# Optimization experiments

Measured on AMD Instinct MI355X. Metric: run time of the kernel, lower is better.

Reference implementation:

```python
import jax, jax.numpy as jnp
import numpy as np

B, N, D, L = 4, 256, 512, 3  # batch, seq_len, input_dim, n_layer


def setup_inputs() -> dict:
    key = jax.random.key(0)
    ks = jax.random.split(key, 12)
    s = 0.02
    return {
        "x": jax.random.normal(ks[0], (B, N, D), dtype=jnp.float32),
        # Highway: L layers, each a gate Linear(D,D) and transform Linear(D,D)
        "hw_gate_w": jax.random.normal(ks[1], (L, D, D), dtype=jnp.float32) * s,
        "hw_gate_b": jnp.zeros((L, D), dtype=jnp.float32),
        "hw_tr_w": jax.random.normal(ks[2], (L, D, D), dtype=jnp.float32) * s,
        "hw_tr_b": jnp.zeros((L, D), dtype=jnp.float32),
        # link_weight MLP: Linear(2D,D) -> ReLU -> [Linear(D,D) -> ReLU]*(L-2) -> Linear(D,1) -> Sigmoid
        "lw0_w": jax.random.normal(ks[3], (D, 2 * D), dtype=jnp.float32) * s,
        "lw0_b": jnp.zeros((D,), dtype=jnp.float32),
        "lw1_w": jax.random.normal(ks[4], (D, D), dtype=jnp.float32) * s,
        "lw1_b": jnp.zeros((D,), dtype=jnp.float32),
        "lwo_w": jax.random.normal(ks[5], (1, D), dtype=jnp.float32) * s,
        "lwo_b": jnp.zeros((1,), dtype=jnp.float32),
    }


def _highway(x, gw, gb, tw, tb):
    # standard highway: y = g * relu(Wt x + bt) + (1 - g) * x, g = sigmoid(Wg x + bg)
    for i in range(gw.shape[0]):
        g = jax.nn.sigmoid(jnp.einsum('bnd,ed->bne', x, gw[i]) + gb[i])
        t = jax.nn.relu(jnp.einsum('bnd,ed->bne', x, tw[i]) + tb[i])
        x = g * t + (1.0 - g) * x
    return x


def reference(x, hw_gate_w, hw_gate_b, hw_tr_w, hw_tr_b,
              lw0_w, lw0_b, lw1_w, lw1_b, lwo_w, lwo_b):
    d = x.shape[-1]
    h = _highway(x, hw_gate_w, hw_gate_b, hw_tr_w, hw_tr_b)  # [B,N,D]
    # Fused pairwise-concat + first Linear: cat(h_i, h_j) @ W0.T ==
    # h_i @ W0[:, :D].T + h_j @ W0[:, D:].T  (avoids the [B,N*N,2D] tensor)
    a = jnp.einsum('bnd,ed->bne', h, lw0_w[:, :d])  # uses m1 (row i)
    b = jnp.einsum('bnd,ed->bne', h, lw0_w[:, d:])  # uses m2 (col j)
    z = jax.nn.relu(a[:, :, None, :] + b[:, None, :, :] + lw0_b)  # [B,N,N,D]
    # (dropout is identity in eval mode)
    z = jax.nn.relu(jnp.einsum('bijd,ed->bije', z, lw1_w) + lw1_b)  # n_layer-2 == 1 hidden layer
    out = jax.nn.sigmoid(jnp.einsum('bijd,d->bij', z, lwo_w[0]) + lwo_b[0])
    return out  # [B,N,N]
```

## Files before the change

kernel.cpp:

```cpp
#include <hip/hip_runtime.h>
#include <hip/hip_bf16.h>

#define BB 4
#define NN 256
#define DD 512

using short8   = __attribute__((ext_vector_type(8))) short;
using f32x4    = __attribute__((ext_vector_type(4))) float;
using uint32x4 = __attribute__((ext_vector_type(4))) unsigned int;

__device__ __forceinline__ unsigned short f2bf(float f) {
    unsigned int u = __float_as_uint(f);
    unsigned int r = (u + 0x7fffu + ((u >> 16) & 1u)) >> 16;
    return (unsigned short)r;
}

__device__ __forceinline__ unsigned cvtpk(float lo, float hi) {
    unsigned r;
    asm("v_cvt_pk_bf16_f32 %0, %1, %2" : "=v"(r) : "v"(lo), "v"(hi));
    return r;
}

template <int ROWS, int NW>
__device__ __forceinline__ void stage_rows(const unsigned short* src, int stride,
                                           short* dst, int tid) {
    int wave = tid >> 6, lane = tid & 63;
#pragma unroll
    for (int c = 0; c < ROWS / (8 * NW); ++c) {
        int rbase = (c * NW + wave) * 8;
        int row   = rbase + (lane >> 3);
        int slot  = (lane & 7) ^ (row & 7);
        const unsigned short* g = src + (size_t)row * stride + slot * 8;
        __builtin_amdgcn_global_load_lds(
            (const __attribute__((address_space(1))) void*)g,
            (__attribute__((address_space(3))) void*)(dst + rbase * 64),
            16, 0, 0);
    }
}

__device__ __forceinline__ short8 read_frag(const short* T, int rowBase, int k2) {
    int lane = threadIdx.x & 63;
    int row  = rowBase + (lane & 15);
    int slot = ((k2 * 4) + (lane >> 4)) ^ (row & 7);
    return *(const short8*)(T + row * 64 + slot * 8);
}

__global__ void prep_kernel(const float* __restrict__ x,
                            const float* __restrict__ gw, const float* __restrict__ tw,
                            const float* __restrict__ w0, const float* __restrict__ w1,
                            float* __restrict__ h0_f32, unsigned short* __restrict__ h0_bf,
                            unsigned short* __restrict__ wg_bf, unsigned short* __restrict__ wt_bf,
                            unsigned short* __restrict__ w0c_bf, unsigned short* __restrict__ w1_bf) {
    const int S_X = BB * NN * DD;
    const int S_W = 3 * DD * DD;
    const int S_W0 = 2 * DD * DD;
    const int S_W1 = DD * DD;
    int total = S_X + S_W + S_W + S_W0 + S_W1;
    for (int idx = blockIdx.x * blockDim.x + threadIdx.x; idx < total;
         idx += gridDim.x * blockDim.x) {
        int t = idx;
        if (t < S_X) { float v = x[t]; h0_f32[t] = v; h0_bf[t] = f2bf(v); continue; }
        t -= S_X;
        if (t < S_W) { wg_bf[t] = f2bf(gw[t]); continue; }
        t -= S_W;
        if (t < S_W) { wt_bf[t] = f2bf(tw[t]); continue; }
        t -= S_W;
        if (t < S_W0) {
            int e = t >> 9, d = t & 511;
            float v = (e < DD) ? w0[e * (2 * DD) + d] : w0[(e - DD) * (2 * DD) + DD + d];
            w0c_bf[t] = f2bf(v); continue;
        }
        t -= S_W0;
        w1_bf[t] = f2bf(w1[t]);
    }
}

__global__ __launch_bounds__(256) void highway_kernel(
        const float* __restrict__ h_in, const unsigned short* __restrict__ hbf_in,
        const unsigned short* __restrict__ wg_bf, const unsigned short* __restrict__ wt_bf,
        const float* __restrict__ gb, const float* __restrict__ tb,
        float* __restrict__ h_out, unsigned short* __restrict__ hbf_out) {
    __shared__ short ht[64 * 64];
    __shared__ short wgt[64 * 64];
    __shared__ short wtt[64 * 64];
    int tid = threadIdx.x, lane = tid & 63, wave = tid >> 6;
    int mt = blockIdx.x >> 3, et = blockIdx.x & 7;
    int m0 = mt * 64, e0 = et * 64;
    int wm = wave >> 1, we = wave & 1;
    f32x4 gacc[2][2] = {}, tacc[2][2] = {};
    for (int ks = 0; ks < 8; ++ks) {
        int d0 = ks * 64;
        __syncthreads();
        stage_rows<64, 4>(hbf_in + (size_t)m0 * DD + d0, DD, ht, tid);
        stage_rows<64, 4>(wg_bf + (size_t)e0 * DD + d0, DD, wgt, tid);
        stage_rows<64, 4>(wt_bf + (size_t)e0 * DD + d0, DD, wtt, tid);
        __syncthreads();
#pragma unroll
        for (int k2 = 0; k2 < 2; ++k2) {
            short8 af[2], bg[2], bt[2];
#pragma unroll
            for (int f = 0; f < 2; ++f) af[f] = read_frag(ht, wm * 32 + f * 16, k2);
#pragma unroll
            for (int f = 0; f < 2; ++f) bg[f] = read_frag(wgt, we * 32 + f * 16, k2);
#pragma unroll
            for (int f = 0; f < 2; ++f) bt[f] = read_frag(wtt, we * 32 + f * 16, k2);
#pragma unroll
            for (int fm = 0; fm < 2; ++fm)
#pragma unroll
                for (int fn = 0; fn < 2; ++fn) {
                    gacc[fm][fn] = __builtin_amdgcn_mfma_f32_16x16x32_bf16(af[fm], bg[fn], gacc[fm][fn], 0, 0, 0);
                    tacc[fm][fn] = __builtin_amdgcn_mfma_f32_16x16x32_bf16(af[fm], bt[fn], tacc[fm][fn], 0, 0, 0);
                }
        }
    }
#pragma unroll
    for (int fm = 0; fm < 2; ++fm)
#pragma unroll
        for (int fn = 0; fn < 2; ++fn) {
            int e = e0 + we * 32 + fn * 16 + (lane & 15);
            float gbe = gb[e], tbe = tb[e];
#pragma unroll
            for (int r = 0; r < 4; ++r) {
                int m = m0 + wm * 32 + fm * 16 + (lane >> 4) * 4 + r;
                float g = 1.f / (1.f + __expf(-(gacc[fm][fn][r] + gbe)));
                float tv = tacc[fm][fn][r] + tbe; tv = tv > 0.f ? tv : 0.f;
                float ho = h_in[(size_t)m * DD + e];
                float hn = g * tv + (1.f - g) * ho;
                h_out[(size_t)m * DD + e] = hn;
                hbf_out[(size_t)m * DD + e] = f2bf(hn);
            }
        }
}

__global__ __launch_bounds__(256) void ab_kernel(
        const unsigned short* __restrict__ hbf, const unsigned short* __restrict__ w0c_bf,
        const float* __restrict__ lw0_b,
        float* __restrict__ a_out, float* __restrict__ b_out) {
    __shared__ short ht[64 * 64];
    __shared__ short wt_[128 * 64];
    int tid = threadIdx.x, lane = tid & 63, wave = tid >> 6;
    int mt = blockIdx.x >> 3, et = blockIdx.x & 7;
    int m0 = mt * 64, e0 = et * 128;
    int wm = wave >> 1, we = wave & 1;
    f32x4 acc[2][4] = {};
    for (int ks = 0; ks < 8; ++ks) {
        __syncthreads();
        stage_rows<64, 4>(hbf + (size_t)m0 * DD + ks * 64, DD, ht, tid);
        stage_rows<128, 4>(w0c_bf + (size_t)e0 * DD + ks * 64, DD, wt_, tid);
        __syncthreads();
#pragma unroll
        for (int k2 = 0; k2 < 2; ++k2) {
            short8 af[2], bf_[4];
#pragma unroll
            for (int f = 0; f < 2; ++f) af[f] = read_frag(ht, wm * 32 + f * 16, k2);
#pragma unroll
            for (int f = 0; f < 4; ++f) bf_[f] = read_frag(wt_, we * 64 + f * 16, k2);
#pragma unroll
            for (int fm = 0; fm < 2; ++fm)
#pragma unroll
                for (int fn = 0; fn < 4; ++fn)
                    acc[fm][fn] = __builtin_amdgcn_mfma_f32_16x16x32_bf16(af[fm], bf_[fn], acc[fm][fn], 0, 0, 0);
        }
    }
#pragma unroll
    for (int fm = 0; fm < 2; ++fm)
#pragma unroll
        for (int fn = 0; fn < 4; ++fn) {
            int e = e0 + we * 64 + fn * 16 + (lane & 15);
#pragma unroll
            for (int r = 0; r < 4; ++r) {
                int m = m0 + wm * 32 + fm * 16 + (lane >> 4) * 4 + r;
                float v = acc[fm][fn][r];
                if (e < DD) a_out[(size_t)m * DD + e] = v + lw0_b[e];
                else        b_out[(size_t)m * DD + (e - DD)] = v;
            }
        }
}


#define Z_LOADS(K)                                                            \
    {                                                                         \
        const int dl_ = (K) * 64 + s * 8;                                     \
        alo = *(const f32x4*)(arow + dl_);                                    \
        ahi = *(const f32x4*)(arow + dl_ + 4);                                \
        const float* b0_ = brow + (size_t)rr * DD + dl_;                      \
        const float* b1_ = brow + (size_t)(64 + rr) * DD + dl_;               \
        b0lo = *(const f32x4*)b0_; b0hi = *(const f32x4*)(b0_ + 4);           \
        b1lo = *(const f32x4*)b1_; b1hi = *(const f32x4*)(b1_ + 4);           \
    }

#define Z_MATH()                                                              \
    {                                                                         \
        zw0[0] = cvtpk(fmaxf(alo[0] + b0lo[0], 0.f), fmaxf(alo[1] + b0lo[1], 0.f)); \
        zw0[1] = cvtpk(fmaxf(alo[2] + b0lo[2], 0.f), fmaxf(alo[3] + b0lo[3], 0.f)); \
        zw0[2] = cvtpk(fmaxf(ahi[0] + b0hi[0], 0.f), fmaxf(ahi[1] + b0hi[1], 0.f)); \
        zw0[3] = cvtpk(fmaxf(ahi[2] + b0hi[2], 0.f), fmaxf(ahi[3] + b0hi[3], 0.f)); \
        zw1[0] = cvtpk(fmaxf(alo[0] + b1lo[0], 0.f), fmaxf(alo[1] + b1lo[1], 0.f)); \
        zw1[1] = cvtpk(fmaxf(alo[2] + b1lo[2], 0.f), fmaxf(alo[3] + b1lo[3], 0.f)); \
        zw1[2] = cvtpk(fmaxf(ahi[0] + b1hi[0], 0.f), fmaxf(ahi[1] + b1hi[1], 0.f)); \
        zw1[3] = cvtpk(fmaxf(ahi[2] + b1hi[2], 0.f), fmaxf(ahi[3] + b1hi[3], 0.f)); \
    }

#define Z_WRITE(BUF)                                                          \
    {                                                                         \
        *(uint32x4*)((BUF) + rr * 64 + ((s ^ (rr & 7)) * 8)) = zw0;           \
        const int r1_ = 64 + rr;                                              \
        *(uint32x4*)((BUF) + r1_ * 64 + ((s ^ (r1_ & 7)) * 8)) = zw1;         \
    }

__global__ __launch_bounds__(512, 2) void pair_kernel(
        const float* __restrict__ a_f32, const float* __restrict__ b_f32,
        const unsigned short* __restrict__ w1_bf,
        const float* __restrict__ lw1_b, const float* __restrict__ lwo_w,
        const float* __restrict__ lwo_b, float* __restrict__ out) {
    __shared__ short ws[2][512 * 64];
    __shared__ short zs[2][128 * 64];
    int tid = threadIdx.x, lane = tid & 63, wave = tid >> 6;
    int bid = blockIdx.x;
    int swz = (bid & 7) * 256 + (bid >> 3);
    int bb = swz >> 9, i = (swz >> 1) & 255, j0 = (swz & 1) * 128;
    const float* arow = a_f32 + (size_t)(bb * NN + i) * DD;
    const float* brow = b_f32 + (size_t)(bb * NN + j0) * DD;
    int s = tid & 7, rr = tid >> 3;
    int we = wave;

    f32x4 acc[8][4] = {};
    uint32x4 zw0, zw1;
    f32x4 alo, ahi, b0lo, b0hi, b1lo, b1hi;

    Z_LOADS(0)
    stage_rows<512, 8>(w1_bf, DD, ws[0], tid);
    Z_MATH()
    Z_WRITE(zs[0])
    asm volatile("s_waitcnt lgkmcnt(0)" ::: "memory");

#pragma unroll
    for (int k = 0; k < 8; ++k) {
        __builtin_amdgcn_s_barrier();
        __builtin_amdgcn_sched_barrier(0);
        if (k < 7) {
            Z_LOADS(k + 1)
            stage_rows<512, 8>(w1_bf + (size_t)(k + 1) * 64, DD, ws[(k + 1) & 1], tid);
            asm volatile("s_waitcnt vmcnt(14)" ::: "memory");
        } else {
            asm volatile("s_waitcnt vmcnt(0)" ::: "memory");
        }
        __builtin_amdgcn_sched_barrier(0);

        const short* zc = zs[k & 1];
        const short* wc = ws[k & 1];
        __builtin_amdgcn_s_setprio(1);
#pragma unroll
        for (int k2 = 0; k2 < 2; ++k2) {
            short8 bfr[4];
#pragma unroll
            for (int f = 0; f < 4; ++f) bfr[f] = read_frag(wc, we * 64 + f * 16, k2);
#pragma unroll
            for (int fh = 0; fh < 2; ++fh) {
                short8 af[4];
#pragma unroll
                for (int f = 0; f < 4; ++f) af[f] = read_frag(zc, (fh * 4 + f) * 16, k2);
#pragma unroll
                for (int fm = 0; fm < 4; ++fm)
#pragma unroll
                    for (int fn = 0; fn < 4; ++fn)
                        acc[fh * 4 + fm][fn] = __builtin_amdgcn_mfma_f32_16x16x32_bf16(
                            af[fm], bfr[fn], acc[fh * 4 + fm][fn], 0, 0, 0);
            }
        }
        __builtin_amdgcn_s_setprio(0);

        if (k < 7) {
            Z_MATH()
            Z_WRITE(zs[(k + 1) & 1])
            asm volatile("s_waitcnt lgkmcnt(0)" ::: "memory");
        }
    }

    __syncthreads();
    float* s_red = (float*)zs;
#pragma unroll
    for (int fm = 0; fm < 8; ++fm) {
        float red[4] = {0.f, 0.f, 0.f, 0.f};
#pragma unroll
        for (int fn = 0; fn < 4; ++fn) {
            int e = we * 64 + fn * 16 + (lane & 15);
            float b1e = lw1_b[e], woe = lwo_w[e];
#pragma unroll
            for (int r = 0; r < 4; ++r) {
                float v = acc[fm][fn][r] + b1e;
                red[r] += (v > 0.f) ? v * woe : 0.f;
            }
        }
#pragma unroll
        for (int mask = 1; mask < 16; mask <<= 1)
#pragma unroll
            for (int r = 0; r < 4; ++r) red[r] += __shfl_xor(red[r], mask, 64);
        if ((lane & 15) == 0) {
#pragma unroll
            for (int r = 0; r < 4; ++r)
                s_red[we * 128 + fm * 16 + (lane >> 4) * 4 + r] = red[r];
        }
    }
    __syncthreads();
    if (tid < 128) {
        float v = lwo_b[0];
#pragma unroll
        for (int w8 = 0; w8 < 8; ++w8) v += s_red[w8 * 128 + tid];
        out[((size_t)(bb * NN + i)) * NN + j0 + tid] = 1.f / (1.f + __expf(-v));
    }
}

extern "C" void kernel_launch(void* const* d_in, const int* in_sizes, int n_in,
                              void* d_out, int out_size, void* d_ws, size_t ws_size,
                              hipStream_t stream) {
    const float* x    = (const float*)d_in[0];
    const float* gw   = (const float*)d_in[1];
    const float* gb   = (const float*)d_in[2];
    const float* tw   = (const float*)d_in[3];
    const float* tb   = (const float*)d_in[4];
    const float* w0   = (const float*)d_in[5];
    const float* w0b  = (const float*)d_in[6];
    const float* w1   = (const float*)d_in[7];
    const float* w1b_ = (const float*)d_in[8];
    const float* wo   = (const float*)d_in[9];
    const float* wob  = (const float*)d_in[10];
    float* out = (float*)d_out;

    char* w = (char*)d_ws;
    float* hA  = (float*)w;            w += (size_t)BB * NN * DD * 4;
    float* hB  = (float*)w;            w += (size_t)BB * NN * DD * 4;
    unsigned short* hbA = (unsigned short*)w; w += (size_t)BB * NN * DD * 2;
    unsigned short* hbB = (unsigned short*)w; w += (size_t)BB * NN * DD * 2;
    float* a_f = (float*)w;            w += (size_t)BB * NN * DD * 4;
    float* b_f = (float*)w;            w += (size_t)BB * NN * DD * 4;
    unsigned short* wg_bf  = (unsigned short*)w; w += (size_t)3 * DD * DD * 2;
    unsigned short* wt_bf  = (unsigned short*)w; w += (size_t)3 * DD * DD * 2;
    unsigned short* w0c_bf = (unsigned short*)w; w += (size_t)2 * DD * DD * 2;
    unsigned short* w1_bf  = (unsigned short*)w; w += (size_t)DD * DD * 2;

    prep_kernel<<<1024, 256, 0, stream>>>(x, gw, tw, w0, w1, hA, hbA, wg_bf, wt_bf, w0c_bf, w1_bf);

    highway_kernel<<<128, 256, 0, stream>>>(hA, hbA, wg_bf + 0 * DD * DD, wt_bf + 0 * DD * DD,
                                            gb + 0 * DD, tb + 0 * DD, hB, hbB);
    highway_kernel<<<128, 256, 0, stream>>>(hB, hbB, wg_bf + 1 * DD * DD, wt_bf + 1 * DD * DD,
                                            gb + 1 * DD, tb + 1 * DD, hA, hbA);
    highway_kernel<<<128, 256, 0, stream>>>(hA, hbA, wg_bf + 2 * DD * DD, wt_bf + 2 * DD * DD,
                                            gb + 2 * DD, tb + 2 * DD, hB, hbB);

    ab_kernel<<<128, 256, 0, stream>>>(hbB, w0c_bf, w0b, a_f, b_f);

    pair_kernel<<<2048, 512, 0, stream>>>(a_f, b_f, w1_bf, w1b_, wo, wob, out);
}
```

Before: 220.3 us.

## Replace double-buffered pipeline with synchronous 128-wide K stages in pair kernel

Drops the software-pipelined double-buffer loop, which prefetched the next K chunk of W1 and z while MFMAs ran on the current one. Each of four iterations now loads two 64-wide K chunks, synchronizes, and computes on both, then reloads. This halves the number of barrier rounds and simplifies waitcnt handling. In exchange, global loads no longer overlap with MFMA work inside a block and must rely on the two co-resident blocks per CU to hide latency.

```diff
diff --git a/kernel.cpp b/kernel.cpp
--- a/kernel.cpp
+++ b/kernel.cpp
@@ -54,8 +54,7 @@
     const int S_X = BB * NN * DD;
     const int S_W = 3 * DD * DD;
     const int S_W0 = 2 * DD * DD;
-    const int S_W1 = DD * DD;
-    int total = S_X + S_W + S_W + S_W0 + S_W1;
+    int total = S_X + S_W + S_W + S_W0 + DD * DD;
     for (int idx = blockIdx.x * blockDim.x + threadIdx.x; idx < total;
          idx += gridDim.x * blockDim.x) {
         int t = idx;
@@ -178,19 +177,18 @@
 }
 
 
-#define Z_LOADS(K)                                                            \
+#define ZPROD(DCOL, BUF)                                                      \
     {                                                                         \
-        const int dl_ = (K) * 64 + s * 8;                                     \
-        alo = *(const f32x4*)(arow + dl_);                                    \
-        ahi = *(const f32x4*)(arow + dl_ + 4);                                \
+        const int dl_ = (DCOL) + s * 8;                                       \
+        f32x4 alo = *(const f32x4*)(arow + dl_);                              \
+        f32x4 ahi = *(const f32x4*)(arow + dl_ + 4);                          \
         const float* b0_ = brow + (size_t)rr * DD + dl_;                      \
         const float* b1_ = brow + (size_t)(64 + rr) * DD + dl_;               \
-        b0lo = *(const f32x4*)b0_; b0hi = *(const f32x4*)(b0_ + 4);           \
-        b1lo = *(const f32x4*)b1_; b1hi = *(const f32x4*)(b1_ + 4);           \
-    }
-
-#define Z_MATH()                                                              \
-    {                                                                         \
+        f32x4 b0lo = *(const f32x4*)b0_;                                      \
+        f32x4 b0hi = *(const f32x4*)(b0_ + 4);                                \
+        f32x4 b1lo = *(const f32x4*)b1_;                                      \
+        f32x4 b1hi = *(const f32x4*)(b1_ + 4);                                \
+        uint32x4 zw0, zw1;                                                    \
         zw0[0] = cvtpk(fmaxf(alo[0] + b0lo[0], 0.f), fmaxf(alo[1] + b0lo[1], 0.f)); \
         zw0[1] = cvtpk(fmaxf(alo[2] + b0lo[2], 0.f), fmaxf(alo[3] + b0lo[3], 0.f)); \
         zw0[2] = cvtpk(fmaxf(ahi[0] + b0hi[0], 0.f), fmaxf(ahi[1] + b0hi[1], 0.f)); \
@@ -199,13 +197,31 @@
         zw1[1] = cvtpk(fmaxf(alo[2] + b1lo[2], 0.f), fmaxf(alo[3] + b1lo[3], 0.f)); \
         zw1[2] = cvtpk(fmaxf(ahi[0] + b1hi[0], 0.f), fmaxf(ahi[1] + b1hi[1], 0.f)); \
         zw1[3] = cvtpk(fmaxf(ahi[2] + b1hi[2], 0.f), fmaxf(ahi[3] + b1hi[3], 0.f)); \
-    }
-
-#define Z_WRITE(BUF)                                                          \
-    {                                                                         \
         *(uint32x4*)((BUF) + rr * 64 + ((s ^ (rr & 7)) * 8)) = zw0;           \
         const int r1_ = 64 + rr;                                              \
         *(uint32x4*)((BUF) + r1_ * 64 + ((s ^ (r1_ & 7)) * 8)) = zw1;         \
+    }
+
+#define HALF_COMPUTE(ZC, WC)                                                  \
+    _Pragma("unroll")                                                         \
+    for (int k2 = 0; k2 < 2; ++k2) {                                          \
+        short8 bfr[4];                                                        \
+        _Pragma("unroll")                                                     \
+        for (int f = 0; f < 4; ++f) bfr[f] = read_frag((WC), we * 64 + f * 16, k2); \
+        _Pragma("unroll")                                                     \
+        for (int fh = 0; fh < 2; ++fh) {                                      \
+            short8 af[4];                                                     \
+            _Pragma("unroll")                                                 \
+            for (int f = 0; f < 4; ++f) af[f] = read_frag((ZC), (fh * 4 + f) * 16, k2); \
+            __builtin_amdgcn_s_setprio(1);                                    \
+            _Pragma("unroll")                                                 \
+            for (int fm = 0; fm < 4; ++fm)                                    \
+                _Pragma("unroll")                                             \
+                for (int fn = 0; fn < 4; ++fn)                                \
+                    acc[fh * 4 + fm][fn] = __builtin_amdgcn_mfma_f32_16x16x32_bf16( \
+                        af[fm], bfr[fn], acc[fh * 4 + fm][fn], 0, 0, 0);      \
+            __builtin_amdgcn_s_setprio(0);                                    \
+        }                                                                     \
     }
 
 __global__ __launch_bounds__(512, 2) void pair_kernel(
@@ -213,8 +229,10 @@
         const unsigned short* __restrict__ w1_bf,
         const float* __restrict__ lw1_b, const float* __restrict__ lwo_w,
         const float* __restrict__ lwo_b, float* __restrict__ out) {
-    __shared__ short ws[2][512 * 64];
-    __shared__ short zs[2][128 * 64];
+    __shared__ short ws0[512 * 64];
+    __shared__ short ws1[512 * 64];
+    __shared__ short z0[128 * 64];
+    __shared__ short z1[128 * 64];
     int tid = threadIdx.x, lane = tid & 63, wave = tid >> 6;
     int bid = blockIdx.x;
     int swz = (bid & 7) * 256 + (bid >> 3);
@@ -225,60 +243,29 @@
     int we = wave;
 
     f32x4 acc[8][4] = {};
-    uint32x4 zw0, zw1;
-    f32x4 alo, ahi, b0lo, b0hi, b1lo, b1hi;
-
-    Z_LOADS(0)
-    stage_rows<512, 8>(w1_bf, DD, ws[0], tid);
-    Z_MATH()
-    Z_WRITE(zs[0])
-    asm volatile("s_waitcnt lgkmcnt(0)" ::: "memory");
-
-#pragma unroll
-    for (int k = 0; k < 8; ++k) {
-        __builtin_amdgcn_s_barrier();
-        __builtin_amdgcn_sched_barrier(0);
-        if (k < 7) {
-            Z_LOADS(k + 1)
-            stage_rows<512, 8>(w1_bf + (size_t)(k + 1) * 64, DD, ws[(k + 1) & 1], tid);
-            asm volatile("s_waitcnt vmcnt(14)" ::: "memory");
-        } else {
-            asm volatile("s_waitcnt vmcnt(0)" ::: "memory");
-        }
-        __builtin_amdgcn_sched_barrier(0);
-
-        const short* zc = zs[k & 1];
-        const short* wc = ws[k & 1];
-        __builtin_amdgcn_s_setprio(1);
-#pragma unroll
-        for (int k2 = 0; k2 < 2; ++k2) {
-            short8 bfr[4];
-#pragma unroll
-            for (int f = 0; f < 4; ++f) bfr[f] = read_frag(wc, we * 64 + f * 16, k2);
-#pragma unroll
-            for (int fh = 0; fh < 2; ++fh) {
-                short8 af[4];
-#pragma unroll
-                for (int f = 0; f < 4; ++f) af[f] = read_frag(zc, (fh * 4 + f) * 16, k2);
-#pragma unroll
-                for (int fm = 0; fm < 4; ++fm)
-#pragma unroll
-                    for (int fn = 0; fn < 4; ++fn)
-                        acc[fh * 4 + fm][fn] = __builtin_amdgcn_mfma_f32_16x16x32_bf16(
-                            af[fm], bfr[fn], acc[fh * 4 + fm][fn], 0, 0, 0);
-            }
-        }
-        __builtin_amdgcn_s_setprio(0);
-
-        if (k < 7) {
-            Z_MATH()
-            Z_WRITE(zs[(k + 1) & 1])
-            asm volatile("s_waitcnt lgkmcnt(0)" ::: "memory");
-        }
-    }
-
+
+    stage_rows<512, 8>(w1_bf, DD, ws0, tid);
+    stage_rows<512, 8>(w1_bf + 64, DD, ws1, tid);
+    ZPROD(0, z0)
+    ZPROD(64, z1)
     __syncthreads();
-    float* s_red = (float*)zs;
+
+#pragma unroll
+    for (int k = 0; k < 4; ++k) {
+        HALF_COMPUTE(z0, ws0)
+        HALF_COMPUTE(z1, ws1)
+        __syncthreads();
+        if (k < 3) {
+            const int d0 = (k + 1) * 128;
+            stage_rows<512, 8>(w1_bf + d0, DD, ws0, tid);
+            stage_rows<512, 8>(w1_bf + d0 + 64, DD, ws1, tid);
+            ZPROD(d0, z0)
+            ZPROD(d0 + 64, z1)
+        }
+        __syncthreads();
+    }
+
+    float* s_red = (float*)z0;
 #pragma unroll
     for (int fm = 0; fm < 8; ++fm) {
         float red[4] = {0.f, 0.f, 0.f, 0.f};
```

New measurement: 261.5 us. 1.19x slower.
